# Optimization experiments

Hardware: AMD Instinct MI355X
Metric: run time of the kernel (lower is better)

Reference implementation:

```python
import jax, jax.numpy as jnp
import numpy as np
import math

D_MODEL = 1024
N_HEADS = 16
HEAD_DIM = D_MODEL // N_HEADS
BAND_RADIUS = 2
BAND_VAL = 0.1


def setup_inputs() -> dict:
    key = jax.random.key(0)
    ks = jax.random.split(key, 12)
    B, S = 4, 2048
    scale = 1.0 / math.sqrt(D_MODEL)
    inp = {
        "x": jax.random.normal(ks[0], (B, S, D_MODEL), dtype=jnp.float32),
        "ocr_context": jax.random.normal(ks[1], (B, S, D_MODEL), dtype=jnp.float32),
        "Wq": jax.random.normal(ks[2], (D_MODEL, D_MODEL), dtype=jnp.float32) * scale,
        "bq": jnp.zeros((D_MODEL,), dtype=jnp.float32),
        "Wk": jax.random.normal(ks[3], (D_MODEL, D_MODEL), dtype=jnp.float32) * scale,
        "bk": jnp.zeros((D_MODEL,), dtype=jnp.float32),
        "Wv": jax.random.normal(ks[4], (D_MODEL, D_MODEL), dtype=jnp.float32) * scale,
        "bv": jnp.zeros((D_MODEL,), dtype=jnp.float32),
        "Wo": jax.random.normal(ks[5], (D_MODEL, D_MODEL), dtype=jnp.float32) * scale,
        "bo": jnp.zeros((D_MODEL,), dtype=jnp.float32),
        "ocr_bias": jax.random.normal(ks[6], (D_MODEL,), dtype=jnp.float32),
    }
    return inp


def _band_mask(S, dtype):
    # additive mask: 0.1 inside |i-j| <= 2, else 0 (matches _create_ocr_pattern_mask)
    i = jnp.arange(S)
    band = (jnp.abs(i[:, None] - i[None, :]) <= BAND_RADIUS).astype(dtype) * BAND_VAL
    return band[None, None, :, :]  # [1,1,S,S], broadcasts over batch & heads


def reference(x, ocr_context, Wq, bq, Wk, bk, Wv, bv, Wo, bo, ocr_bias):
    B, S, _ = x.shape
    # torch Linear: x @ W.T + b
    q = x @ Wq.T + bq + ocr_bias  # ocr bias added to q before head split
    k = x @ Wk.T + bk
    v = x @ Wv.T + bv
    q = q.reshape(B, S, N_HEADS, HEAD_DIM).transpose(0, 2, 1, 3)  # [B,H,S,d]
    k = k.reshape(B, S, N_HEADS, HEAD_DIM).transpose(0, 2, 1, 3)
    v = v.reshape(B, S, N_HEADS, HEAD_DIM).transpose(0, 2, 1, 3)
    scores = jnp.einsum("bhsd,bhtd->bhst", q, k) / math.sqrt(HEAD_DIM)
    scores = scores + _band_mask(S, scores.dtype)  # ocr_context only supplies shape
    attn = jax.nn.softmax(scores, axis=-1)
    out = jnp.einsum("bhst,bhtd->bhsd", attn, v)
    out = out.transpose(0, 2, 1, 3).reshape(B, S, D_MODEL)
    return out @ Wo.T + bo
```

## Files before the change

### kernel.cpp

```cpp
#include <hip/hip_runtime.h>
#include <hip/hip_bf16.h>
#include <stdint.h>

typedef __attribute__((ext_vector_type(8))) short bf16x8;
typedef __attribute__((ext_vector_type(4))) float f32x4;
typedef __attribute__((ext_vector_type(16))) float f32x16;
typedef __attribute__((ext_vector_type(4))) unsigned u32x4;

#define L2E 1.4426950408889634f

static __device__ __forceinline__ unsigned short f2bf(float f) {
    __hip_bfloat16 h = __float2bfloat16(f);
    return __builtin_bit_cast(unsigned short, h);
}

static __device__ __forceinline__ void gl2lds16(const void* g, void* l) {
    __builtin_amdgcn_global_load_lds(
        (const __attribute__((address_space(1))) void*)g,
        (__attribute__((address_space(3))) void*)l,
        16, 0, 0);
}

__global__ void cast_kernel(const float* __restrict__ src,
                            unsigned short* __restrict__ dst, int n4) {
    int i = blockIdx.x * blockDim.x + threadIdx.x;
    int stride = gridDim.x * blockDim.x;
    for (; i < n4; i += stride) {
        float4 v = ((const float4*)src)[i];
        ushort4 o;
        o.x = f2bf(v.x); o.y = f2bf(v.y); o.z = f2bf(v.z); o.w = f2bf(v.w);
        ((ushort4*)dst)[i] = o;
    }
}

__global__ void cast4_kernel(const float* __restrict__ s0, const float* __restrict__ s1,
                             const float* __restrict__ s2, const float* __restrict__ s3,
                             unsigned short* __restrict__ d0, unsigned short* __restrict__ d1,
                             unsigned short* __restrict__ d2, unsigned short* __restrict__ d3) {
    const int m = blockIdx.y;
    const float* src = m == 0 ? s0 : m == 1 ? s1 : m == 2 ? s2 : s3;
    unsigned short* dst = m == 0 ? d0 : m == 1 ? d1 : m == 2 ? d2 : d3;
    int i = blockIdx.x * blockDim.x + threadIdx.x;
    for (; i < 262144; i += 256 * 256) {
        float4 v = ((const float4*)src)[i];
        ushort4 o;
        o.x = f2bf(v.x); o.y = f2bf(v.y); o.z = f2bf(v.z); o.w = f2bf(v.w);
        ((ushort4*)dst)[i] = o;
    }
}

__global__ __launch_bounds__(256) void qkv_gemm(
    const unsigned short* __restrict__ A,
    const unsigned short* __restrict__ Wq,
    const unsigned short* __restrict__ Wk,
    const unsigned short* __restrict__ Wv,
    const float* __restrict__ bq,
    const float* __restrict__ bk,
    const float* __restrict__ bv,
    const float* __restrict__ ocr,
    float qscale,
    unsigned short* __restrict__ Qo,
    unsigned short* __restrict__ Ko,
    unsigned short* __restrict__ VTo)
{
    constexpr int K = 1024;
    __shared__ unsigned short As[128][64];
    __shared__ unsigned short Bs[128][64];

    const int tid  = threadIdx.x;
    const int wave = tid >> 6, lane = tid & 63;
    const int li = lane & 15, lg = lane >> 4;

    const int lin = blockIdx.y * 24 + blockIdx.x;
    const int n2  = (lin & 7) * 192 + (lin >> 3);
    const int mb = n2 / 24, nbb = n2 - mb * 24;
    const int proj = nbb >> 3;
    const int m0 = mb * 128, n0 = (nbb & 7) * 128;

    const unsigned short* W = proj == 0 ? Wq : proj == 1 ? Wk : Wv;
    const float* bias = proj == 0 ? bq : proj == 1 ? bk : bv;

    const int wm = (wave >> 1) * 64, wn = (wave & 1) * 64;
    const int srow = wave * 8 + (lane >> 3);
    const int scol = (lane & 7) * 8;

    f32x4 acc[4][4] = {};

    for (int k0 = 0; k0 < K; k0 += 64) {
#pragma unroll
        for (int rnd = 0; rnd < 4; ++rnd)
            gl2lds16(A + (size_t)(m0 + rnd * 32 + srow) * K + k0 + scol,
                     &As[rnd * 32 + wave * 8][0]);
#pragma unroll
        for (int rnd = 0; rnd < 4; ++rnd)
            gl2lds16(W + (size_t)(n0 + rnd * 32 + srow) * K + k0 + scol,
                     &Bs[rnd * 32 + wave * 8][0]);
        __syncthreads();
#pragma unroll
        for (int kk = 0; kk < 64; kk += 32) {
            bf16x8 af[4], bfr[4];
#pragma unroll
            for (int m = 0; m < 4; ++m)
                af[m] = *(const bf16x8*)&As[wm + m * 16 + li][kk + lg * 8];
#pragma unroll
            for (int n = 0; n < 4; ++n)
                bfr[n] = *(const bf16x8*)&Bs[wn + n * 16 + li][kk + lg * 8];
#pragma unroll
            for (int m = 0; m < 4; ++m)
#pragma unroll
                for (int n = 0; n < 4; ++n)
                    acc[m][n] = __builtin_amdgcn_mfma_f32_16x16x32_bf16(
                        af[m], bfr[n], acc[m][n], 0, 0, 0);
        }
        __syncthreads();
    }

    const float scale = proj == 0 ? qscale : 1.f;
#pragma unroll
    for (int n = 0; n < 4; ++n) {
        const int col = n0 + wn + n * 16 + li;
        float bb = bias[col];
        if (proj == 0) bb += ocr[col];
#pragma unroll
        for (int m = 0; m < 4; ++m) {
            if (proj == 2) {
                const int row0 = m0 + wm + m * 16 + lg * 4;
                size_t addr = ((size_t)(((row0 >> 11) << 4) + (col >> 6)) * 64 + (col & 63)) * 2048
                              + (row0 & 2047);
                ushort4 o;
                o.x = f2bf(acc[m][n][0] + bb);
                o.y = f2bf(acc[m][n][1] + bb);
                o.z = f2bf(acc[m][n][2] + bb);
                o.w = f2bf(acc[m][n][3] + bb);
                *(ushort4*)&VTo[addr] = o;
            } else {
                unsigned short* dst = proj == 0 ? Qo : Ko;
#pragma unroll
                for (int r = 0; r < 4; ++r) {
                    const int row = m0 + wm + m * 16 + lg * 4 + r;
                    dst[(size_t)row * 1024 + col] = f2bf((acc[m][n][r] + bb) * scale);
                }
            }
        }
    }
}

__global__ __launch_bounds__(256) void out_gemm(
    const unsigned short* __restrict__ A,
    const unsigned short* __restrict__ W,
    const float* __restrict__ bias,
    float* __restrict__ of)
{
    constexpr int K = 1024;
    __shared__ unsigned short As[128][64];
    __shared__ unsigned short Bs[128][64];

    const int tid  = threadIdx.x;
    const int wave = tid >> 6, lane = tid & 63;
    const int li = lane & 15, lg = lane >> 4;
    const int lin = blockIdx.y * 8 + blockIdx.x;
    const int n2  = (lin & 7) * 64 + (lin >> 3);
    const int m0 = (n2 >> 3) * 128, n0 = (n2 & 7) * 128;
    const int wm = (wave >> 1) * 64, wn = (wave & 1) * 64;

    const int srow = wave * 8 + (lane >> 3);
    const int scol = (lane & 7) * 8;

    f32x4 acc[4][4] = {};

    for (int k0 = 0; k0 < K; k0 += 64) {
#pragma unroll
        for (int rnd = 0; rnd < 4; ++rnd)
            gl2lds16(A + (size_t)(m0 + rnd * 32 + srow) * K + k0 + scol,
                     &As[rnd * 32 + wave * 8][0]);
#pragma unroll
        for (int rnd = 0; rnd < 4; ++rnd)
            gl2lds16(W + (size_t)(n0 + rnd * 32 + srow) * K + k0 + scol,
                     &Bs[rnd * 32 + wave * 8][0]);
        __syncthreads();
#pragma unroll
        for (int kk = 0; kk < 64; kk += 32) {
            bf16x8 af[4], bfr[4];
#pragma unroll
            for (int m = 0; m < 4; ++m)
                af[m] = *(const bf16x8*)&As[wm + m * 16 + li][kk + lg * 8];
#pragma unroll
            for (int n = 0; n < 4; ++n)
                bfr[n] = *(const bf16x8*)&Bs[wn + n * 16 + li][kk + lg * 8];
#pragma unroll
            for (int m = 0; m < 4; ++m)
#pragma unroll
                for (int n = 0; n < 4; ++n)
                    acc[m][n] = __builtin_amdgcn_mfma_f32_16x16x32_bf16(
                        af[m], bfr[n], acc[m][n], 0, 0, 0);
        }
        __syncthreads();
    }

#pragma unroll
    for (int n = 0; n < 4; ++n) {
        const int col = n0 + wn + n * 16 + li;
        const float bb = bias[col];
#pragma unroll
        for (int m = 0; m < 4; ++m)
#pragma unroll
            for (int r = 0; r < 4; ++r) {
                const int row = m0 + wm + m * 16 + lg * 4 + r;
                of[(size_t)row * 1024 + col] = acc[m][n][r] + bb;
            }
    }
}

__global__ __launch_bounds__(256, 4) void attn_kernel(
    const unsigned short* __restrict__ Q,
    const unsigned short* __restrict__ Km,
    const unsigned short* __restrict__ VT,
    unsigned short* __restrict__ AO)
{
    __shared__ unsigned short Ks[2][4096];
    __shared__ unsigned short Vs[2][4096];

    const int tid  = threadIdx.x;
    const int w = tid >> 6, lane = tid & 63;
    const int li5 = lane & 31, l5 = lane >> 5, li7 = li5 & 7;

    const int p  = blockIdx.y * 16 + blockIdx.x;
    const int q_ = (p & 7) * 128 + (p >> 3);
    const int bx = q_ & 15, bh = q_ >> 4;
    const int b = bh >> 4, h = bh & 15;
    const int qb = bx * 128 + w * 32;
    const int qrow = qb + li5;

    const int srow = w * 16 + (lane >> 3);
    const int swz  = ((lane & 7) ^ (lane >> 3)) * 8;

    const unsigned short* Kg0 = Km + (size_t)(b * 2048 + srow) * 1024 + h * 64 + swz;
    const unsigned short* Vg0 = VT + ((size_t)bh * 64 + srow) * 2048 + swz;

    bf16x8 qf[4];
#pragma unroll
    for (int f = 0; f < 4; ++f)
        qf[f] = *(const bf16x8*)&Q[(size_t)(b * 2048 + qrow) * 1024 + h * 64
                                   + f * 16 + l5 * 8];

    f32x16 acc[2] = {};
    float ls0 = 0.f, ls1 = 0.f, ls2 = 0.f, ls3 = 0.f;

#pragma unroll
    for (int it = 0; it < 2; ++it) {
        gl2lds16(Kg0 + (size_t)(it * 8) * 1024, &Ks[0][(w * 2 + it) * 512]);
        gl2lds16(Vg0 + (size_t)(it * 8) * 2048, &Vs[0][(w * 2 + it) * 512]);
    }
    __syncthreads();

    for (int t = 0; t < 32; ++t) {
        const int buf = t & 1;
        const int j0 = t * 64;
        if (t < 31) {
            const int j1 = j0 + 64;
#pragma unroll
            for (int it = 0; it < 2; ++it) {
                gl2lds16(Kg0 + (size_t)(j1 + it * 8) * 1024, &Ks[buf ^ 1][(w * 2 + it) * 512]);
                gl2lds16(Vg0 + (size_t)(it * 8) * 2048 + j1, &Vs[buf ^ 1][(w * 2 + it) * 512]);
            }
        }

        f32x16 st[2];
        __builtin_amdgcn_s_setprio(1);
#pragma unroll
        for (int jf = 0; jf < 2; ++jf) {
            f32x16 z = {};
#pragma unroll
            for (int f = 0; f < 4; ++f) {
                bf16x8 kf = *(const bf16x8*)&Ks[buf][(jf * 32 + li5) * 64
                                                     + ((f * 2 + l5) ^ li7) * 8];
                z = __builtin_amdgcn_mfma_f32_32x32x16_bf16(kf, qf[f], z, 0, 0, 0);
            }
            st[jf] = z;
        }
        __builtin_amdgcn_s_setprio(0);

        if (j0 >= qb - 65 && j0 <= qb + 33) {
#pragma unroll
            for (int jf = 0; jf < 2; ++jf)
#pragma unroll
                for (int r = 0; r < 16; ++r) {
                    int j = j0 + jf * 32 + (r & 3) + 8 * (r >> 2) + 4 * l5;
                    int dq = qrow - j;
                    if ((unsigned)(dq + 2) <= 4u) st[jf][r] += 0.1f * L2E;
                }
        }

        unsigned pw[2][8];
#pragma unroll
        for (int jf = 0; jf < 2; ++jf) {
#pragma unroll
            for (int m = 0; m < 8; ++m) {
                float p0 = __builtin_amdgcn_exp2f(st[jf][2 * m]);
                float p1 = __builtin_amdgcn_exp2f(st[jf][2 * m + 1]);
                if (m == 0) { ls0 += p0; ls1 += p1; }
                else if (m == 1) { ls2 += p0; ls3 += p1; }
                else if (m == 2) { ls0 += p0; ls1 += p1; }
                else if (m == 3) { ls2 += p0; ls3 += p1; }
                else if (m == 4) { ls0 += p0; ls1 += p1; }
                else if (m == 5) { ls2 += p0; ls3 += p1; }
                else if (m == 6) { ls0 += p0; ls1 += p1; }
                else             { ls2 += p0; ls3 += p1; }
                asm("v_cvt_pk_bf16_f32 %0, %1, %2"
                    : "=v"(pw[jf][m]) : "v"(p0), "v"(p1));
            }
        }

#pragma unroll
        for (int jf = 0; jf < 2; ++jf)
#pragma unroll
            for (int m2 = 0; m2 < 2; ++m2)
#pragma unroll
                for (int m0_ = 0; m0_ < 2; ++m0_) {
                    unsigned a0 = pw[jf][m2 * 4 + m0_];
                    unsigned b0 = pw[jf][m2 * 4 + m0_ + 2];
                    asm volatile("v_permlane32_swap_b32 %0, %1"
                                 : "+v"(a0), "+v"(b0));
                    pw[jf][m2 * 4 + m0_]     = a0;
                    pw[jf][m2 * 4 + m0_ + 2] = b0;
                }

        __builtin_amdgcn_s_setprio(1);
#pragma unroll
        for (int db = 0; db < 2; ++db)
#pragma unroll
            for (int tt = 0; tt < 4; ++tt) {
                bf16x8 vf = *(const bf16x8*)&Vs[buf][(db * 32 + li5) * 64
                                                     + ((tt * 2 + l5) ^ li7) * 8];
                const int jf = tt >> 1, m2 = tt & 1;
                u32x4 tw = {pw[jf][m2 * 4 + 0], pw[jf][m2 * 4 + 1],
                            pw[jf][m2 * 4 + 2], pw[jf][m2 * 4 + 3]};
                acc[db] = __builtin_amdgcn_mfma_f32_32x32x16_bf16(
                    vf, __builtin_bit_cast(bf16x8, tw), acc[db], 0, 0, 0);
            }
        __builtin_amdgcn_s_setprio(0);
        __syncthreads();
    }

    float lr = (ls0 + ls1) + (ls2 + ls3);
    float l2 = lr + __shfl_xor(lr, 32);
    const float inv = 1.f / l2;
#pragma unroll
    for (int db = 0; db < 2; ++db)
#pragma unroll
        for (int g = 0; g < 4; ++g) {
            ushort4 o;
            o.x = f2bf(acc[db][g * 4 + 0] * inv);
            o.y = f2bf(acc[db][g * 4 + 1] * inv);
            o.z = f2bf(acc[db][g * 4 + 2] * inv);
            o.w = f2bf(acc[db][g * 4 + 3] * inv);
            *(ushort4*)&AO[(size_t)(b * 2048 + qrow) * 1024 + h * 64
                           + db * 32 + g * 8 + l5 * 4] = o;
        }
}

extern "C" void kernel_launch(void* const* d_in, const int* in_sizes, int n_in,
                              void* d_out, int out_size, void* d_ws, size_t ws_size,
                              hipStream_t stream) {
    const float* x   = (const float*)d_in[0];
    const float* Wq  = (const float*)d_in[2];
    const float* bq  = (const float*)d_in[3];
    const float* Wk  = (const float*)d_in[4];
    const float* bk  = (const float*)d_in[5];
    const float* Wv  = (const float*)d_in[6];
    const float* bv  = (const float*)d_in[7];
    const float* Wo  = (const float*)d_in[8];
    const float* bo  = (const float*)d_in[9];
    const float* ocr = (const float*)d_in[10];
    float* out = (float*)d_out;

    char* ws = (char*)d_ws;
    const size_t MB = 1024 * 1024;
    unsigned short* xb  = (unsigned short*)(ws);
    unsigned short* Wqb = (unsigned short*)(ws + 16 * MB);
    unsigned short* Wkb = (unsigned short*)(ws + 18 * MB);
    unsigned short* Wvb = (unsigned short*)(ws + 20 * MB);
    unsigned short* Wob = (unsigned short*)(ws + 22 * MB);
    unsigned short* Qb  = (unsigned short*)(ws + 24 * MB);
    unsigned short* Kb  = (unsigned short*)(ws + 40 * MB);
    unsigned short* VTb = (unsigned short*)(ws + 56 * MB);
    unsigned short* AO  = xb;

    cast_kernel<<<2048, 256, 0, stream>>>(x, xb, 8388608 / 4);
    cast4_kernel<<<dim3(256, 4), 256, 0, stream>>>(Wq, Wk, Wv, Wo,
                                                   Wqb, Wkb, Wvb, Wob);

    const float QSC = 0.125f * L2E;
    qkv_gemm<<<dim3(24, 64), 256, 0, stream>>>(xb, Wqb, Wkb, Wvb,
                                               bq, bk, bv, ocr, QSC,
                                               Qb, Kb, VTb);

    attn_kernel<<<dim3(16, 64), 256, 0, stream>>>(Qb, Kb, VTb, AO);

    out_gemm<<<dim3(8, 64), 256, 0, stream>>>(AO, Wob, bo, out);
}
```

Before: 197.6 us.

## Process two 32-row query subtiles per wave to reuse K/V fragments

Each wave now handles 64 query rows (two 32-row subtiles) instead of 32, so K fragments read from LDS are held in registers and reused across both subtiles, and each V fragment feeds two MFMAs. The grid is halved to 512 blocks and launch bounds drop to 2 blocks per SM to allow the larger register footprint. This cuts LDS traffic and global K/V loads per query row but lowers occupancy and the number of blocks available to fill the GPU.

```diff
diff --git a/kernel.cpp b/kernel.cpp
--- a/kernel.cpp
+++ b/kernel.cpp
@@ -211,7 +211,7 @@
     }
 }
 
-__global__ __launch_bounds__(256, 4) void attn_kernel(
+__global__ __launch_bounds__(256, 2) void attn_kernel(
     const unsigned short* __restrict__ Q,
     const unsigned short* __restrict__ Km,
     const unsigned short* __restrict__ VT,
@@ -224,12 +224,11 @@
     const int w = tid >> 6, lane = tid & 63;
     const int li5 = lane & 31, l5 = lane >> 5, li7 = li5 & 7;
 
-    const int p  = blockIdx.y * 16 + blockIdx.x;
-    const int q_ = (p & 7) * 128 + (p >> 3);
-    const int bx = q_ & 15, bh = q_ >> 4;
+    const int p  = blockIdx.y * 8 + blockIdx.x;
+    const int q_ = (p & 7) * 64 + (p >> 3);
+    const int bx = q_ & 7, bh = q_ >> 3;
     const int b = bh >> 4, h = bh & 15;
-    const int qb = bx * 128 + w * 32;
-    const int qrow = qb + li5;
+    const int qb = bx * 256 + w * 64;
 
     const int srow = w * 16 + (lane >> 3);
     const int swz  = ((lane & 7) ^ (lane >> 3)) * 8;
@@ -237,14 +236,16 @@
     const unsigned short* Kg0 = Km + (size_t)(b * 2048 + srow) * 1024 + h * 64 + swz;
     const unsigned short* Vg0 = VT + ((size_t)bh * 64 + srow) * 2048 + swz;
 
-    bf16x8 qf[4];
-#pragma unroll
-    for (int f = 0; f < 4; ++f)
-        qf[f] = *(const bf16x8*)&Q[(size_t)(b * 2048 + qrow) * 1024 + h * 64
-                                   + f * 16 + l5 * 8];
-
-    f32x16 acc[2] = {};
-    float ls0 = 0.f, ls1 = 0.f, ls2 = 0.f, ls3 = 0.f;
+    bf16x8 qf[2][4];
+#pragma unroll
+    for (int s = 0; s < 2; ++s)
+#pragma unroll
+        for (int f = 0; f < 4; ++f)
+            qf[s][f] = *(const bf16x8*)&Q[(size_t)(b * 2048 + qb + s * 32 + li5) * 1024
+                                          + h * 64 + f * 16 + l5 * 8];
+
+    f32x16 acc[2][2] = {};
+    float ls00 = 0.f, ls01 = 0.f, ls10 = 0.f, ls11 = 0.f;
 
 #pragma unroll
     for (int it = 0; it < 2; ++it) {
@@ -265,65 +266,68 @@
             }
         }
 
-        f32x16 st[2];
-        __builtin_amdgcn_s_setprio(1);
-#pragma unroll
-        for (int jf = 0; jf < 2; ++jf) {
-            f32x16 z = {};
-#pragma unroll
-            for (int f = 0; f < 4; ++f) {
-                bf16x8 kf = *(const bf16x8*)&Ks[buf][(jf * 32 + li5) * 64
+        bf16x8 kf[2][4];
+#pragma unroll
+        for (int jf = 0; jf < 2; ++jf)
+#pragma unroll
+            for (int f = 0; f < 4; ++f)
+                kf[jf][f] = *(const bf16x8*)&Ks[buf][(jf * 32 + li5) * 64
                                                      + ((f * 2 + l5) ^ li7) * 8];
-                z = __builtin_amdgcn_mfma_f32_32x32x16_bf16(kf, qf[f], z, 0, 0, 0);
-            }
-            st[jf] = z;
+
+        unsigned pw[2][2][8];
+#pragma unroll
+        for (int s = 0; s < 2; ++s) {
+            f32x16 st[2];
+            __builtin_amdgcn_s_setprio(1);
+#pragma unroll
+            for (int jf = 0; jf < 2; ++jf) {
+                f32x16 z = {};
+#pragma unroll
+                for (int f = 0; f < 4; ++f)
+                    z = __builtin_amdgcn_mfma_f32_32x32x16_bf16(kf[jf][f], qf[s][f], z, 0, 0, 0);
+                st[jf] = z;
+            }
+            __builtin_amdgcn_s_setprio(0);
+
+            const int qbs = qb + s * 32;
+            if (j0 >= qbs - 65 && j0 <= qbs + 33) {
+#pragma unroll
+                for (int jf = 0; jf < 2; ++jf)
+#pragma unroll
+                    for (int r = 0; r < 16; ++r) {
+                        int j = j0 + jf * 32 + (r & 3) + 8 * (r >> 2) + 4 * l5;
+                        int dq = (qbs + li5) - j;
+                        if ((unsigned)(dq + 2) <= 4u) st[jf][r] += 0.1f * L2E;
+                    }
+            }
+
+#pragma unroll
+            for (int jf = 0; jf < 2; ++jf)
+#pragma unroll
+                for (int m = 0; m < 8; ++m) {
+                    float p0 = __builtin_amdgcn_exp2f(st[jf][2 * m]);
+                    float p1 = __builtin_amdgcn_exp2f(st[jf][2 * m + 1]);
+                    float pp = p0 + p1;
+                    if (s == 0) { if (m & 1) ls01 += pp; else ls00 += pp; }
+                    else        { if (m & 1) ls11 += pp; else ls10 += pp; }
+                    asm("v_cvt_pk_bf16_f32 %0, %1, %2"
+                        : "=v"(pw[s][jf][m]) : "v"(p0), "v"(p1));
+                }
+
+#pragma unroll
+            for (int jf = 0; jf < 2; ++jf)
+#pragma unroll
+                for (int m2 = 0; m2 < 2; ++m2)
+#pragma unroll
+                    for (int m0_ = 0; m0_ < 2; ++m0_) {
+                        unsigned a0 = pw[s][jf][m2 * 4 + m0_];
+                        unsigned b0 = pw[s][jf][m2 * 4 + m0_ + 2];
+                        asm volatile("v_permlane32_swap_b32 %0, %1"
+                                     : "+v"(a0), "+v"(b0));
+                        pw[s][jf][m2 * 4 + m0_]     = a0;
+                        pw[s][jf][m2 * 4 + m0_ + 2] = b0;
+                    }
         }
-        __builtin_amdgcn_s_setprio(0);
-
-        if (j0 >= qb - 65 && j0 <= qb + 33) {
-#pragma unroll
-            for (int jf = 0; jf < 2; ++jf)
-#pragma unroll
-                for (int r = 0; r < 16; ++r) {
-                    int j = j0 + jf * 32 + (r & 3) + 8 * (r >> 2) + 4 * l5;
-                    int dq = qrow - j;
-                    if ((unsigned)(dq + 2) <= 4u) st[jf][r] += 0.1f * L2E;
-                }
-        }
-
-        unsigned pw[2][8];
-#pragma unroll
-        for (int jf = 0; jf < 2; ++jf) {
-#pragma unroll
-            for (int m = 0; m < 8; ++m) {
-                float p0 = __builtin_amdgcn_exp2f(st[jf][2 * m]);
-                float p1 = __builtin_amdgcn_exp2f(st[jf][2 * m + 1]);
-                if (m == 0) { ls0 += p0; ls1 += p1; }
-                else if (m == 1) { ls2 += p0; ls3 += p1; }
-                else if (m == 2) { ls0 += p0; ls1 += p1; }
-                else if (m == 3) { ls2 += p0; ls3 += p1; }
-                else if (m == 4) { ls0 += p0; ls1 += p1; }
-                else if (m == 5) { ls2 += p0; ls3 += p1; }
-                else if (m == 6) { ls0 += p0; ls1 += p1; }
-                else             { ls2 += p0; ls3 += p1; }
-                asm("v_cvt_pk_bf16_f32 %0, %1, %2"
-                    : "=v"(pw[jf][m]) : "v"(p0), "v"(p1));
-            }
-        }
-
-#pragma unroll
-        for (int jf = 0; jf < 2; ++jf)
-#pragma unroll
-            for (int m2 = 0; m2 < 2; ++m2)
-#pragma unroll
-                for (int m0_ = 0; m0_ < 2; ++m0_) {
-                    unsigned a0 = pw[jf][m2 * 4 + m0_];
-                    unsigned b0 = pw[jf][m2 * 4 + m0_ + 2];
-                    asm volatile("v_permlane32_swap_b32 %0, %1"
-                                 : "+v"(a0), "+v"(b0));
-                    pw[jf][m2 * 4 + m0_]     = a0;
-                    pw[jf][m2 * 4 + m0_ + 2] = b0;
-                }
 
         __builtin_amdgcn_s_setprio(1);
 #pragma unroll
@@ -333,30 +337,37 @@
                 bf16x8 vf = *(const bf16x8*)&Vs[buf][(db * 32 + li5) * 64
                                                      + ((tt * 2 + l5) ^ li7) * 8];
                 const int jf = tt >> 1, m2 = tt & 1;
-                u32x4 tw = {pw[jf][m2 * 4 + 0], pw[jf][m2 * 4 + 1],
-                            pw[jf][m2 * 4 + 2], pw[jf][m2 * 4 + 3]};
-                acc[db] = __builtin_amdgcn_mfma_f32_32x32x16_bf16(
-                    vf, __builtin_bit_cast(bf16x8, tw), acc[db], 0, 0, 0);
+#pragma unroll
+                for (int s = 0; s < 2; ++s) {
+                    u32x4 tw = {pw[s][jf][m2 * 4 + 0], pw[s][jf][m2 * 4 + 1],
+                                pw[s][jf][m2 * 4 + 2], pw[s][jf][m2 * 4 + 3]};
+                    acc[s][db] = __builtin_amdgcn_mfma_f32_32x32x16_bf16(
+                        vf, __builtin_bit_cast(bf16x8, tw), acc[s][db], 0, 0, 0);
+                }
             }
         __builtin_amdgcn_s_setprio(0);
         __syncthreads();
     }
 
-    float lr = (ls0 + ls1) + (ls2 + ls3);
-    float l2 = lr + __shfl_xor(lr, 32);
-    const float inv = 1.f / l2;
-#pragma unroll
-    for (int db = 0; db < 2; ++db)
-#pragma unroll
-        for (int g = 0; g < 4; ++g) {
-            ushort4 o;
-            o.x = f2bf(acc[db][g * 4 + 0] * inv);
-            o.y = f2bf(acc[db][g * 4 + 1] * inv);
-            o.z = f2bf(acc[db][g * 4 + 2] * inv);
-            o.w = f2bf(acc[db][g * 4 + 3] * inv);
-            *(ushort4*)&AO[(size_t)(b * 2048 + qrow) * 1024 + h * 64
-                           + db * 32 + g * 8 + l5 * 4] = o;
-        }
+#pragma unroll
+    for (int s = 0; s < 2; ++s) {
+        float lr = s == 0 ? (ls00 + ls01) : (ls10 + ls11);
+        float l2 = lr + __shfl_xor(lr, 32);
+        const float inv = 1.f / l2;
+        const int qrow = qb + s * 32 + li5;
+#pragma unroll
+        for (int db = 0; db < 2; ++db)
+#pragma unroll
+            for (int g = 0; g < 4; ++g) {
+                ushort4 o;
+                o.x = f2bf(acc[s][db][g * 4 + 0] * inv);
+                o.y = f2bf(acc[s][db][g * 4 + 1] * inv);
+                o.z = f2bf(acc[s][db][g * 4 + 2] * inv);
+                o.w = f2bf(acc[s][db][g * 4 + 3] * inv);
+                *(ushort4*)&AO[(size_t)(b * 2048 + qrow) * 1024 + h * 64
+                               + db * 32 + g * 8 + l5 * 4] = o;
+            }
+    }
 }
 
 extern "C" void kernel_launch(void* const* d_in, const int* in_sizes, int n_in,
@@ -395,7 +406,7 @@
                                                bq, bk, bv, ocr, QSC,
                                                Qb, Kb, VTb);
 
-    attn_kernel<<<dim3(16, 64), 256, 0, stream>>>(Qb, Kb, VTb, AO);
+    attn_kernel<<<dim3(8, 64), 256, 0, stream>>>(Qb, Kb, VTb, AO);
 
     out_gemm<<<dim3(8, 64), 256, 0, stream>>>(AO, Wob, bo, out);
 }
```

New measurement: 193.3 us. -2.2%, faster.
